# Kernel optimization log

Hardware: AMD Instinct MI355X
Metric: run time of the kernel (lower is better)

Reference implementation:

```python
import jax, jax.numpy as jnp
import numpy as np

# Configuration mirroring init_kwargs
B, H, W = 64, 40, 40          # batch, grid (image 1280 / stride 32)
A, C = 5, 80                  # anchors per cell, classes
MAX_BOXES = 100               # max_detection_boxes
SCORE_THR = 0.001             # nms_score_threshold
IOU_THR = 0.5                 # nms_iou_threshold


def setup_inputs() -> dict:
    key = jax.random.key(0)
    k1, k2 = jax.random.split(key)
    predictions = jax.random.normal(k1, (B, H, W, A * (5 + C)), dtype=jnp.float32)
    # anchor (w, h) in grid-cell units, positive
    anchors = jax.random.uniform(k2, (A, 2), dtype=jnp.float32, minval=0.5, maxval=8.0)
    return {"predictions": predictions, "anchors": anchors}


def decode_yolo(predictions, anchors):
    """YOLOv2-style decode -> normalized corner boxes and per-class scores."""
    b, h, w, _ = predictions.shape
    p = predictions.reshape(b, h, w, A, 5 + C)
    gy, gx = jnp.meshgrid(jnp.arange(h, dtype=jnp.float32),
                          jnp.arange(w, dtype=jnp.float32), indexing="ij")
    grid = jnp.stack([gx, gy], axis=-1)[None, :, :, None, :]   # [1,h,w,1,2]
    dims = jnp.array([w, h], dtype=jnp.float32)
    xy = (jax.nn.sigmoid(p[..., 0:2]) + grid) / dims           # normalized centers
    wh = jnp.exp(p[..., 2:4]) * anchors / dims                 # normalized sizes
    conf = jax.nn.sigmoid(p[..., 4:5])
    probs = jax.nn.softmax(p[..., 5:], axis=-1)
    scores = conf * probs                                      # [b,h,w,A,C]
    boxes = jnp.concatenate([xy - wh * 0.5, xy + wh * 0.5], axis=-1)  # x1,y1,x2,y2
    return boxes.reshape(b, -1, 4), scores.reshape(b, -1, C)


def nms_single(boxes, scores_all):
    """Greedy per-class NMS for one image. boxes [N,4], scores_all [N,C]."""
    cls_scores = jnp.max(scores_all, axis=-1)
    classes = jnp.argmax(scores_all, axis=-1)
    s0 = jnp.where(cls_scores > SCORE_THR, cls_scores, -1.0)
    area = jnp.maximum(boxes[:, 2] - boxes[:, 0], 0.0) * \
           jnp.maximum(boxes[:, 3] - boxes[:, 1], 0.0)

    def step(s, _):
        idx = jnp.argmax(s)
        sc = s[idx]
        box = boxes[idx]
        x1 = jnp.maximum(box[0], boxes[:, 0]); y1 = jnp.maximum(box[1], boxes[:, 1])
        x2 = jnp.minimum(box[2], boxes[:, 2]); y2 = jnp.minimum(box[3], boxes[:, 3])
        inter = jnp.maximum(x2 - x1, 0.0) * jnp.maximum(y2 - y1, 0.0)
        box_area = jnp.maximum(box[2] - box[0], 0.0) * jnp.maximum(box[3] - box[1], 0.0)
        iou = inter / (area + box_area - inter + 1e-8)
        suppress = (iou > IOU_THR) & (classes == classes[idx])
        s_new = jnp.where(suppress, -1.0, s).at[idx].set(-1.0)
        valid = sc > 0.0
        out_box = jnp.where(valid, box, 0.0)
        out_sc = jnp.where(valid, sc, 0.0)
        out_cl = jnp.where(valid, classes[idx], -1)
        return s_new, (out_box, out_sc, out_cl)

    _, (ob, osc, ocl) = jax.lax.scan(step, s0, None, length=MAX_BOXES)
    return ob, osc, ocl  # [MAX_BOXES,4], [MAX_BOXES], [MAX_BOXES]


def reference(predictions, anchors):
    boxes, scores = decode_yolo(predictions, anchors)
    sel_boxes, sel_scores, sel_classes = jax.vmap(nms_single)(boxes, scores)
    return sel_boxes, sel_scores, sel_classes
```

## Files before the change

kernel.cpp:

```cpp
#include <hip/hip_runtime.h>
#include <math.h>

#define B 64
#define H 40
#define W 40
#define A 5
#define C 80
#define NBOX (H*W*A)
#define FEAT (5+C)
#define MAXB 100
#define SCORE_THR 0.001f
#define IOU_THR 0.5f

#define DEC_BOXES 128
#define DEC_THREADS 128

#define SEL_THREADS 1024
#define NWAVES (SEL_THREADS/64)
#define HBINS 10240
#define BINBASE 119808
#define TARGET 512

#define BK 48
#define RCAP 1024

typedef unsigned long long u64;
typedef unsigned int u32;

__global__ __launch_bounds__(DEC_THREADS) void decode_kernel(
    const float* __restrict__ pred, const float* __restrict__ anchors,
    float* __restrict__ boxes_ws, float* __restrict__ s_ws, int* __restrict__ cls_ws)
{
    __shared__ float lds[DEC_BOXES * FEAT];
    const int blk = blockIdx.x;
    const int tid = threadIdx.x;
    const long long base_box = (long long)blk * DEC_BOXES;

    const float4* src = (const float4*)(pred + base_box * FEAT);
    float4* dst = (float4*)lds;
    const int n4 = DEC_BOXES * FEAT / 4;
    for (int i = tid; i < n4; i += DEC_THREADS) dst[i] = src[i];
    __syncthreads();

    const int box = (int)base_box + tid;
    const float* l = lds + tid * FEAT;

    int n    = box % NBOX;
    int cell = n / A;
    int a    = n - cell * A;
    int gx   = cell % W;
    int gy   = cell / W;

    float tx = l[0], ty = l[1], tw = l[2], th = l[3], tc = l[4];

    float lg[C];
    #pragma unroll
    for (int i = 0; i < C; ++i) lg[i] = l[5+i];

    float sx = 1.f / (1.f + expf(-tx));
    float sy = 1.f / (1.f + expf(-ty));
    float cx = (sx + (float)gx) / (float)W;
    float cy = (sy + (float)gy) / (float)H;
    float aw = anchors[a*2+0], ah = anchors[a*2+1];
    float bw = expf(tw) * aw / (float)W;
    float bh = expf(th) * ah / (float)H;
    float conf = 1.f / (1.f + expf(-tc));

    float mm[8];
    #pragma unroll
    for (int w = 0; w < 8; ++w) mm[w] = lg[w];
    #pragma unroll
    for (int i = 8; i < C; ++i) mm[i & 7] = fmaxf(mm[i & 7], lg[i]);
    float m = fmaxf(fmaxf(fmaxf(mm[0],mm[1]),fmaxf(mm[2],mm[3])),
                    fmaxf(fmaxf(mm[4],mm[5]),fmaxf(mm[6],mm[7])));

    float sum = 0.f;
    float bv[4] = {-1.f,-1.f,-1.f,-1.f};
    int   bi[4] = {0,0,0,0};
    #pragma unroll
    for (int i = 0; i < C; ++i) {
        float e = expf(lg[i] - m);
        sum += e;
        int w = i & 3;
        if (e > bv[w]) { bv[w] = e; bi[w] = i; }
    }
    float best_e = bv[0]; int best_c = bi[0];
    #pragma unroll
    for (int w = 1; w < 4; ++w) {
        if (bv[w] > best_e || (bv[w] == best_e && bi[w] < best_c)) { best_e = bv[w]; best_c = bi[w]; }
    }

    float score = conf * (best_e / sum);
    float s0 = (score > SCORE_THR) ? score : -1.0f;

    float x1 = cx - bw*0.5f, y1 = cy - bh*0.5f;
    float x2 = cx + bw*0.5f, y2 = cy + bh*0.5f;

    ((float4*)boxes_ws)[box] = make_float4(x1, y1, x2, y2);
    s_ws[box] = s0;
    cls_ws[box] = best_c;
}

__global__ __launch_bounds__(SEL_THREADS) void select_kernel(
    const float* __restrict__ boxes_ws, const float* __restrict__ s_ws,
    const int* __restrict__ cls_ws,
    int* __restrict__ bucketCnt, u64* __restrict__ bucketKey,
    float4* __restrict__ bucketBox)
{
    __shared__ int hist[HBINS];
    __shared__ int wavesum[NWAVES];
    __shared__ int tbin_s;

    const int img  = blockIdx.x;
    const int tid  = threadIdx.x;
    const int lane = tid & 63;
    const int wid  = tid >> 6;
    const float* bws = boxes_ws + (long long)img * NBOX * 4;
    const float* sws = s_ws     + (long long)img * NBOX;
    const int*   cws = cls_ws   + (long long)img * NBOX;

    #pragma unroll
    for (int q = 0; q < HBINS/SEL_THREADS; ++q) hist[tid + q*SEL_THREADS] = 0;
    if (tid < C)  bucketCnt[img*C + tid] = 0;
    if (tid == 0) tbin_s = 0;
    __syncthreads();

    float sc_r[8];
    #pragma unroll
    for (int k = 0; k < 8; ++k) {
        int j = tid + k*SEL_THREADS;
        float s = (j < NBOX) ? sws[j] : -1.f;
        sc_r[k] = s;
        if (s > 0.f) {
            int b = (int)(__float_as_uint(s) >> 13) - BINBASE;
            b = max(0, min(HBINS-1, b));
            atomicAdd(&hist[b], 1);
        }
    }
    __syncthreads();

    int sum_r = 0;
    {
        int base = HBINS - 10*(tid+1);
        #pragma unroll
        for (int q = 0; q < 10; ++q) sum_r += hist[base + q];
    }
    int incl = sum_r;
    #pragma unroll
    for (int off = 1; off < 64; off <<= 1) {
        int o = __shfl_up(incl, off);
        if (lane >= off) incl += o;
    }
    if (lane == 63) wavesum[wid] = incl;
    __syncthreads();
    {
        int wbase = 0;
        for (int w = 0; w < wid; ++w) wbase += wavesum[w];
        int excl = wbase + incl - sum_r;
        if (excl < TARGET && excl + sum_r >= TARGET) {
            int cum = excl;
            for (int q = 0; q < 10; ++q) {
                int b = HBINS - 10*tid - 1 - q;
                cum += hist[b];
                if (cum >= TARGET) { tbin_s = b; break; }
            }
        }
    }
    __syncthreads();
    const int tb = tbin_s;

    #pragma unroll
    for (int k = 0; k < 8; ++k) {
        int j = tid + k*SEL_THREADS;
        float s = sc_r[k];
        if (j < NBOX && s > 0.f) {
            int b = (int)(__float_as_uint(s) >> 13) - BINBASE;
            b = max(0, min(HBINS-1, b));
            if (b >= tb) {
                int c  = cws[j];
                int bb = img*C + c;
                int pos = atomicAdd(&bucketCnt[bb], 1);
                if (pos < BK) {
                    u64 key = ((u64)__float_as_uint(s) << 32)
                            | ((u64)(NBOX - j) << 19)
                            | ((u64)pos << 13) | (u64)c;
                    bucketKey[bb*BK + pos] = key;
                    bucketBox[bb*BK + pos] = ((const float4*)bws)[j];
                }
            }
        }
    }
}

__device__ __forceinline__ u64 wave_max_u64(u64 v) {
    #define STAGE(CTRL, RMASK) { \
        u32 lo = (u32)v, hi = (u32)(v >> 32); \
        u32 tlo = (u32)__builtin_amdgcn_update_dpp(0, (int)lo, CTRL, RMASK, 0xf, true); \
        u32 thi = (u32)__builtin_amdgcn_update_dpp(0, (int)hi, CTRL, RMASK, 0xf, true); \
        u64 t = ((u64)thi << 32) | (u64)tlo; \
        if (t > v) v = t; \
    }
    STAGE(0x111, 0xf)
    STAGE(0x112, 0xf)
    STAGE(0x114, 0xf)
    STAGE(0x118, 0xf)
    STAGE(0x142, 0xa)
    STAGE(0x143, 0xc)
    #undef STAGE
    u32 flo = (u32)__builtin_amdgcn_readlane((int)(u32)v, 63);
    u32 fhi = (u32)__builtin_amdgcn_readlane((int)(v >> 32), 63);
    return ((u64)fhi << 32) | (u64)flo;
}

__global__ __launch_bounds__(64) void classnms_kernel(
    const int* __restrict__ bucketCnt, const u64* __restrict__ bucketKey,
    const float4* __restrict__ bucketBox, u64* __restrict__ survOut)
{
    const int img  = blockIdx.y;
    const int bb   = img*C + blockIdx.x;
    const int lane = threadIdx.x;
    const int n = min(bucketCnt[bb], BK);

    u64 key = 0, keep = 0;
    float x1=0.f, y1=0.f, x2=0.f, y2=0.f, ar=0.f;
    if (lane < n) {
        key = bucketKey[bb*BK + lane];
        float4 b4 = bucketBox[bb*BK + lane];
        x1=b4.x; y1=b4.y; x2=b4.z; y2=b4.w;
        ar = fmaxf(x2-x1,0.f)*fmaxf(y2-y1,0.f);
    }

    for (int t = 0; t < BK; ++t) {
        u64 bk = wave_max_u64(key);
        if (bk == 0) break;
        int sl = (int)((bk >> 13) & 63);
        float sx1 = __shfl(x1, sl), sy1 = __shfl(y1, sl);
        float sx2 = __shfl(x2, sl), sy2 = __shfl(y2, sl);
        float sarea = fmaxf(sx2-sx1,0.f)*fmaxf(sy2-sy1,0.f);

        if (lane == sl) {
            keep = key;
            key = 0;
        } else if (key != 0) {
            float ix1 = fmaxf(sx1, x1);
            float iy1 = fmaxf(sy1, y1);
            float ix2 = fminf(sx2, x2);
            float iy2 = fminf(sy2, y2);
            float inter = fmaxf(ix2-ix1,0.f)*fmaxf(iy2-iy1,0.f);
            float iou = inter / (ar + sarea - inter + 1e-8f);
            if (iou > IOU_THR) key = 0;
        }
    }

    if (lane < BK) survOut[bb*BK + lane] = keep;
}

__global__ __launch_bounds__(256) void rank_kernel(
    const u64* __restrict__ survOut, const float4* __restrict__ bucketBox,
    float* __restrict__ out)
{
    __shared__ u64 ckeys[RCAP];
    __shared__ int cnt;
    const int img = blockIdx.x;
    const int tid = threadIdx.x;

    if (tid == 0) cnt = 0;
    __syncthreads();

    for (int i = tid; i < C*BK; i += 256) {
        u64 k = survOut[(long long)img*C*BK + i];
        if (k != 0) {
            int p = atomicAdd(&cnt, 1);
            if (p < RCAP) ckeys[p] = k;
        }
    }
    __syncthreads();
    const int m = min(cnt, RCAP);

    float* out_boxes  = out;
    float* out_scores = out + B*MAXB*4;
    float* out_cls    = out + B*MAXB*5;

    for (int i = tid; i < m; i += 256) {
        u64 mine = ckeys[i];
        int r = 0;
        for (int j = 0; j < m; ++j) r += (ckeys[j] > mine) ? 1 : 0;
        if (r < MAXB) {
            int c   = (int)(mine & 127);
            int pos = (int)((mine >> 13) & 63);
            float4 b4 = bucketBox[((long long)img*C + c)*BK + pos];
            int o = img*MAXB + r;
            out_boxes[o*4+0] = b4.x; out_boxes[o*4+1] = b4.y;
            out_boxes[o*4+2] = b4.z; out_boxes[o*4+3] = b4.w;
            out_scores[o] = __uint_as_float((u32)(mine >> 32));
            out_cls[o]    = (float)c;
        }
    }

    int base = min(m, MAXB);
    for (int r = base + tid; r < MAXB; r += 256) {
        int o = img*MAXB + r;
        out_boxes[o*4+0]=0.f; out_boxes[o*4+1]=0.f;
        out_boxes[o*4+2]=0.f; out_boxes[o*4+3]=0.f;
        out_scores[o]=0.f;
        out_cls[o]=-1.f;
    }
}

extern "C" void kernel_launch(void* const* d_in, const int* in_sizes, int n_in,
                              void* d_out, int out_size, void* d_ws, size_t ws_size,
                              hipStream_t stream) {
    const float* pred    = (const float*)d_in[0];
    const float* anchors = (const float*)d_in[1];
    float* out = (float*)d_out;

    char* p = (char*)d_ws;
    float*  boxes_ws  = (float*)p;              p += (size_t)B*NBOX*4*sizeof(float);
    float*  s_ws      = (float*)p;              p += (size_t)B*NBOX*sizeof(float);
    int*    cls_ws    = (int*)p;                p += (size_t)B*NBOX*sizeof(int);
    int*    bucketCnt = (int*)p;                p += (size_t)B*C*sizeof(int);
    u64*    bucketKey = (u64*)p;                p += (size_t)B*C*BK*sizeof(u64);
    u64*    survOut   = (u64*)p;                p += (size_t)B*C*BK*sizeof(u64);
    float4* bucketBox = (float4*)p;

    decode_kernel<<<(B*NBOX)/DEC_BOXES, DEC_THREADS, 0, stream>>>(
        pred, anchors, boxes_ws, s_ws, cls_ws);
    select_kernel<<<B, SEL_THREADS, 0, stream>>>(
        boxes_ws, s_ws, cls_ws, bucketCnt, bucketKey, bucketBox);
    classnms_kernel<<<dim3(C, B), 64, 0, stream>>>(
        bucketCnt, bucketKey, bucketBox, survOut);
    rank_kernel<<<B, 256, 0, stream>>>(
        survOut, bucketBox, out);
}
```

Measured before the change: 342.4 us.

## Stage decode input through small padded LDS chunks into registers

The decode kernel used to copy the whole 128-box tile (about 43KB) into LDS. It now loops over six 16-feature column chunks, staging each chunk in a 17-float padded LDS buffer and pulling the values into registers, and it adds a launch_bounds occupancy hint of 4 blocks. The aim is to cut LDS use so more blocks can be resident, and to avoid bank conflicts when each thread reads its row with an 85-float stride. In exchange the global loads become scalar and strided instead of float4, the kernel adds 12 barriers, and registers may spill.

Result: no change. 339.2 us (-0.9%).

```diff
diff --git a/kernel.cpp b/kernel.cpp
--- a/kernel.cpp
+++ b/kernel.cpp
@@ -14,6 +14,7 @@
 
 #define DEC_BOXES 128
 #define DEC_THREADS 128
+#define DEC_PAD 17
 
 #define SEL_THREADS 1024
 #define NWAVES (SEL_THREADS/64)
@@ -27,35 +28,55 @@
 typedef unsigned long long u64;
 typedef unsigned int u32;
 
-__global__ __launch_bounds__(DEC_THREADS) void decode_kernel(
+__global__ __launch_bounds__(DEC_THREADS, 4) void decode_kernel(
     const float* __restrict__ pred, const float* __restrict__ anchors,
     float* __restrict__ boxes_ws, float* __restrict__ s_ws, int* __restrict__ cls_ws)
 {
-    __shared__ float lds[DEC_BOXES * FEAT];
+    __shared__ float lds[DEC_BOXES * DEC_PAD];
     const int blk = blockIdx.x;
     const int tid = threadIdx.x;
-    const long long base_box = (long long)blk * DEC_BOXES;
-
-    const float4* src = (const float4*)(pred + base_box * FEAT);
-    float4* dst = (float4*)lds;
-    const int n4 = DEC_BOXES * FEAT / 4;
-    for (int i = tid; i < n4; i += DEC_THREADS) dst[i] = src[i];
-    __syncthreads();
-
-    const int box = (int)base_box + tid;
-    const float* l = lds + tid * FEAT;
-
+    const int base_box = blk * DEC_BOXES;
+    const long long tile  = (long long)base_box * FEAT;
+    const long long LIMIT = (long long)B * NBOX * FEAT - 1;
+
+    float v[FEAT];
+
+    #pragma unroll
+    for (int c = 0; c < 6; ++c) {
+        #pragma unroll
+        for (int hh = 0; hh < 2; ++hh) {
+            float stg[8];
+            int   la[8];
+            #pragma unroll
+            for (int s = 0; s < 8; ++s) {
+                int idx = tid + (hh*8 + s) * DEC_THREADS;
+                int b = idx >> 4;
+                int k = idx & 15;
+                long long src = tile + (long long)b * FEAT + c*16 + k;
+                if (src > LIMIT) src = LIMIT;
+                stg[s] = pred[src];
+                la[s]  = b * DEC_PAD + k;
+            }
+            #pragma unroll
+            for (int s = 0; s < 8; ++s) lds[la[s]] = stg[s];
+        }
+        __syncthreads();
+        #pragma unroll
+        for (int j = 0; j < 16; ++j) {
+            int f = c*16 + j;
+            if (f < FEAT) v[f] = lds[tid * DEC_PAD + j];
+        }
+        __syncthreads();
+    }
+
+    const int box = base_box + tid;
     int n    = box % NBOX;
     int cell = n / A;
     int a    = n - cell * A;
     int gx   = cell % W;
     int gy   = cell / W;
 
-    float tx = l[0], ty = l[1], tw = l[2], th = l[3], tc = l[4];
-
-    float lg[C];
-    #pragma unroll
-    for (int i = 0; i < C; ++i) lg[i] = l[5+i];
+    float tx = v[0], ty = v[1], tw = v[2], th = v[3], tc = v[4];
 
     float sx = 1.f / (1.f + expf(-tx));
     float sy = 1.f / (1.f + expf(-ty));
@@ -68,9 +89,9 @@
 
     float mm[8];
     #pragma unroll
-    for (int w = 0; w < 8; ++w) mm[w] = lg[w];
-    #pragma unroll
-    for (int i = 8; i < C; ++i) mm[i & 7] = fmaxf(mm[i & 7], lg[i]);
+    for (int w = 0; w < 8; ++w) mm[w] = v[5+w];
+    #pragma unroll
+    for (int i = 8; i < C; ++i) mm[i & 7] = fmaxf(mm[i & 7], v[5+i]);
     float m = fmaxf(fmaxf(fmaxf(mm[0],mm[1]),fmaxf(mm[2],mm[3])),
                     fmaxf(fmaxf(mm[4],mm[5]),fmaxf(mm[6],mm[7])));
 
@@ -79,7 +100,7 @@
     int   bi[4] = {0,0,0,0};
     #pragma unroll
     for (int i = 0; i < C; ++i) {
-        float e = expf(lg[i] - m);
+        float e = expf(v[5+i] - m);
         sum += e;
         int w = i & 3;
         if (e > bv[w]) { bv[w] = e; bi[w] = i; }
```

## Split per-image select into global histogram, scan, and grid-wide scatter kernels

Applied to the files above, without the earlier changes.

Moves histogram construction into the decode kernel using global atomics and splits the old one-block-per-image select kernel into a small scan kernel and a scatter kernel launched across the whole grid. This spreads the select work, which previously ran on only 64 blocks, over many more threads. It also halves the decode block size. The cost is a memset, an extra kernel launch, and global atomic contention on the histogram.

Result: no change. 341.7 us (-0.2%).

```diff
diff --git a/kernel.cpp b/kernel.cpp
--- a/kernel.cpp
+++ b/kernel.cpp
@@ -12,11 +12,9 @@
 #define SCORE_THR 0.001f
 #define IOU_THR 0.5f
 
-#define DEC_BOXES 128
-#define DEC_THREADS 128
-
-#define SEL_THREADS 1024
-#define NWAVES (SEL_THREADS/64)
+#define DEC_BOXES 64
+#define DEC_THREADS 64
+
 #define HBINS 10240
 #define BINBASE 119808
 #define TARGET 512
@@ -29,23 +27,25 @@
 
 __global__ __launch_bounds__(DEC_THREADS) void decode_kernel(
     const float* __restrict__ pred, const float* __restrict__ anchors,
-    float* __restrict__ boxes_ws, float* __restrict__ s_ws, int* __restrict__ cls_ws)
+    float* __restrict__ boxes_ws, float* __restrict__ s_ws, int* __restrict__ cls_ws,
+    int* __restrict__ ghist)
 {
     __shared__ float lds[DEC_BOXES * FEAT];
     const int blk = blockIdx.x;
     const int tid = threadIdx.x;
-    const long long base_box = (long long)blk * DEC_BOXES;
-
-    const float4* src = (const float4*)(pred + base_box * FEAT);
+    const int base_box = blk * DEC_BOXES;
+
+    const float4* src = (const float4*)(pred + (long long)base_box * FEAT);
     float4* dst = (float4*)lds;
     const int n4 = DEC_BOXES * FEAT / 4;
     for (int i = tid; i < n4; i += DEC_THREADS) dst[i] = src[i];
     __syncthreads();
 
-    const int box = (int)base_box + tid;
+    const int box = base_box + tid;
     const float* l = lds + tid * FEAT;
 
-    int n    = box % NBOX;
+    int img  = box / NBOX;
+    int n    = box - img * NBOX;
     int cell = n / A;
     int a    = n - cell * A;
     int gx   = cell % W;
@@ -99,51 +99,34 @@
     ((float4*)boxes_ws)[box] = make_float4(x1, y1, x2, y2);
     s_ws[box] = s0;
     cls_ws[box] = best_c;
-}
-
-__global__ __launch_bounds__(SEL_THREADS) void select_kernel(
-    const float* __restrict__ boxes_ws, const float* __restrict__ s_ws,
-    const int* __restrict__ cls_ws,
-    int* __restrict__ bucketCnt, u64* __restrict__ bucketKey,
-    float4* __restrict__ bucketBox)
-{
-    __shared__ int hist[HBINS];
-    __shared__ int wavesum[NWAVES];
+
+    if (s0 > 0.f) {
+        int b = (int)(__float_as_uint(s0) >> 13) - BINBASE;
+        b = max(0, min(HBINS-1, b));
+        atomicAdd(&ghist[img*HBINS + b], 1);
+    }
+}
+
+__global__ __launch_bounds__(1024) void scan_kernel(
+    const int* __restrict__ ghist, int* __restrict__ tbin, int* __restrict__ bucketCnt)
+{
+    __shared__ int wavesum[16];
     __shared__ int tbin_s;
-
     const int img  = blockIdx.x;
     const int tid  = threadIdx.x;
     const int lane = tid & 63;
     const int wid  = tid >> 6;
-    const float* bws = boxes_ws + (long long)img * NBOX * 4;
-    const float* sws = s_ws     + (long long)img * NBOX;
-    const int*   cws = cls_ws   + (long long)img * NBOX;
-
-    #pragma unroll
-    for (int q = 0; q < HBINS/SEL_THREADS; ++q) hist[tid + q*SEL_THREADS] = 0;
+    const int* gh = ghist + img * HBINS;
+
     if (tid < C)  bucketCnt[img*C + tid] = 0;
     if (tid == 0) tbin_s = 0;
-    __syncthreads();
-
-    float sc_r[8];
-    #pragma unroll
-    for (int k = 0; k < 8; ++k) {
-        int j = tid + k*SEL_THREADS;
-        float s = (j < NBOX) ? sws[j] : -1.f;
-        sc_r[k] = s;
-        if (s > 0.f) {
-            int b = (int)(__float_as_uint(s) >> 13) - BINBASE;
-            b = max(0, min(HBINS-1, b));
-            atomicAdd(&hist[b], 1);
-        }
-    }
     __syncthreads();
 
     int sum_r = 0;
     {
         int base = HBINS - 10*(tid+1);
         #pragma unroll
-        for (int q = 0; q < 10; ++q) sum_r += hist[base + q];
+        for (int q = 0; q < 10; ++q) sum_r += gh[base + q];
     }
     int incl = sum_r;
     #pragma unroll
@@ -161,34 +144,38 @@
             int cum = excl;
             for (int q = 0; q < 10; ++q) {
                 int b = HBINS - 10*tid - 1 - q;
-                cum += hist[b];
+                cum += gh[b];
                 if (cum >= TARGET) { tbin_s = b; break; }
             }
         }
     }
     __syncthreads();
-    const int tb = tbin_s;
-
-    #pragma unroll
-    for (int k = 0; k < 8; ++k) {
-        int j = tid + k*SEL_THREADS;
-        float s = sc_r[k];
-        if (j < NBOX && s > 0.f) {
-            int b = (int)(__float_as_uint(s) >> 13) - BINBASE;
-            b = max(0, min(HBINS-1, b));
-            if (b >= tb) {
-                int c  = cws[j];
-                int bb = img*C + c;
-                int pos = atomicAdd(&bucketCnt[bb], 1);
-                if (pos < BK) {
-                    u64 key = ((u64)__float_as_uint(s) << 32)
-                            | ((u64)(NBOX - j) << 19)
-                            | ((u64)pos << 13) | (u64)c;
-                    bucketKey[bb*BK + pos] = key;
-                    bucketBox[bb*BK + pos] = ((const float4*)bws)[j];
-                }
-            }
-        }
+    if (tid == 0) tbin[img] = tbin_s;
+}
+
+__global__ __launch_bounds__(256) void scatter_kernel(
+    const float* __restrict__ boxes_ws, const float* __restrict__ s_ws,
+    const int* __restrict__ cls_ws, const int* __restrict__ tbin,
+    int* __restrict__ bucketCnt, u64* __restrict__ bucketKey,
+    float4* __restrict__ bucketBox)
+{
+    const int j = blockIdx.x * 256 + threadIdx.x;
+    float s = s_ws[j];
+    if (s <= 0.f) return;
+    int img = j / NBOX;
+    int b = (int)(__float_as_uint(s) >> 13) - BINBASE;
+    b = max(0, min(HBINS-1, b));
+    if (b < tbin[img]) return;
+    int n  = j - img * NBOX;
+    int c  = cls_ws[j];
+    int bb = img*C + c;
+    int pos = atomicAdd(&bucketCnt[bb], 1);
+    if (pos < BK) {
+        u64 key = ((u64)__float_as_uint(s) << 32)
+                | ((u64)(NBOX - n) << 19)
+                | ((u64)pos << 13) | (u64)c;
+        bucketKey[bb*BK + pos] = key;
+        bucketBox[bb*BK + pos] = ((const float4*)boxes_ws)[j];
     }
 }
 
@@ -321,12 +308,16 @@
     int*    bucketCnt = (int*)p;                p += (size_t)B*C*sizeof(int);
     u64*    bucketKey = (u64*)p;                p += (size_t)B*C*BK*sizeof(u64);
     u64*    survOut   = (u64*)p;                p += (size_t)B*C*BK*sizeof(u64);
-    float4* bucketBox = (float4*)p;
-
+    float4* bucketBox = (float4*)p;             p += (size_t)B*C*BK*sizeof(float4);
+    int*    ghist     = (int*)p;                p += (size_t)B*HBINS*sizeof(int);
+    int*    tbin      = (int*)p;
+
+    hipMemsetAsync(ghist, 0, (size_t)B*HBINS*sizeof(int), stream);
     decode_kernel<<<(B*NBOX)/DEC_BOXES, DEC_THREADS, 0, stream>>>(
-        pred, anchors, boxes_ws, s_ws, cls_ws);
-    select_kernel<<<B, SEL_THREADS, 0, stream>>>(
-        boxes_ws, s_ws, cls_ws, bucketCnt, bucketKey, bucketBox);
+        pred, anchors, boxes_ws, s_ws, cls_ws, ghist);
+    scan_kernel<<<B, 1024, 0, stream>>>(ghist, tbin, bucketCnt);
+    scatter_kernel<<<(B*NBOX)/256, 256, 0, stream>>>(
+        boxes_ws, s_ws, cls_ws, tbin, bucketCnt, bucketKey, bucketBox);
     classnms_kernel<<<dim3(C, B), 64, 0, stream>>>(
         bucketCnt, bucketKey, bucketBox, survOut);
     rank_kernel<<<B, 256, 0, stream>>>(
```
